# Kernel optimization log

Measured on AMD Instinct MI355X. Metric: run time of the kernel, lower is better.

The kernel has to match this reference:

```python
import jax, jax.numpy as jnp
import numpy as np

EMBED = 1024
FF = 4096
LN_EPS = 1e-5

def _layernorm(x, gamma, beta):
    mu = jnp.mean(x, axis=-1, keepdims=True)
    var = jnp.var(x, axis=-1, keepdims=True)
    return (x - mu) * jax.lax.rsqrt(var + LN_EPS) * gamma + beta

def setup_inputs() -> dict:
    key = jax.random.key(0)
    ks = jax.random.split(key, 16)
    s = 1.0 / np.sqrt(EMBED)
    s2 = 1.0 / np.sqrt(FF)
    return {
        "x": jax.random.normal(ks[0], (8, 2048, EMBED), dtype=jnp.float32),
        "Wq": jax.random.uniform(ks[1], (EMBED, EMBED), jnp.float32, -s, s),
        "bq": jnp.zeros((EMBED,), jnp.float32),
        "Wk": jax.random.uniform(ks[2], (EMBED, EMBED), jnp.float32, -s, s),
        "bk": jnp.zeros((EMBED,), jnp.float32),
        "Wv": jax.random.uniform(ks[3], (EMBED, EMBED), jnp.float32, -s, s),
        "bv": jnp.zeros((EMBED,), jnp.float32),
        "Wo": jax.random.uniform(ks[4], (EMBED, EMBED), jnp.float32, -s, s),
        "bo": jnp.zeros((EMBED,), jnp.float32),
        "g1": jnp.ones((EMBED,), jnp.float32),
        "b1": jnp.zeros((EMBED,), jnp.float32),
        "g2": jnp.ones((EMBED,), jnp.float32),
        "b2": jnp.zeros((EMBED,), jnp.float32),
        "W1": jax.random.uniform(ks[5], (EMBED, FF), jnp.float32, -s, s),
        "bf1": jnp.zeros((FF,), jnp.float32),
        "W2": jax.random.uniform(ks[6], (FF, EMBED), jnp.float32, -s2, s2),
        "bf2": jnp.zeros((EMBED,), jnp.float32),
    }

def reference(x, Wq, bq, Wk, bk, Wv, bv, Wo, bo, g1, b1, g2, b2, W1, bf1, W2, bf2):
    # Single-head attention (heads arg unused in original forward)
    Q = jnp.einsum('bse,ef->bsf', x, Wq) + bq
    K = jnp.einsum('bse,ef->bsf', x, Wk) + bk
    V = jnp.einsum('bse,ef->bsf', x, Wv) + bv
    scale = 1.0 / jnp.sqrt(jnp.float32(EMBED))
    scores = jnp.einsum('bqe,bke->bqk', Q, K) * scale  # [B,S,S]
    attn = jax.nn.softmax(scores, axis=-1)
    attn_out = jnp.einsum('bqk,bke->bqe', attn, V)
    attn_out = jnp.einsum('bse,ef->bsf', attn_out, Wo) + bo
    # dropout is identity in eval mode
    h = _layernorm(x + attn_out, g1, b1)
    ffn = jnp.einsum('bsf,fh->bsh', jax.nn.relu(jnp.einsum('bse,eh->bsh', h, W1) + bf1), W2) + bf2
    return _layernorm(h + ffn, g2, b2)
```

## Files before the change

### kernel.cpp

```cpp
#include <hip/hip_runtime.h>


typedef __attribute__((ext_vector_type(4))) float  f32x4;
typedef __attribute__((ext_vector_type(8))) short  s16x8;
typedef __attribute__((ext_vector_type(4))) short  s16x4;
typedef unsigned short u16;
typedef unsigned int   u32;

__device__ __forceinline__ float bf2f(short s) {
  u32 u = ((u32)(u16)s) << 16;
  float f; __builtin_memcpy(&f, &u, 4); return f;
}
__device__ __forceinline__ short f2bf(float f) {
  u32 u; __builtin_memcpy(&u, &f, 4);
  u32 r = (u + 0x7fffu + ((u >> 16) & 1u)) >> 16;
  return (short)(u16)r;
}

__device__ __forceinline__ void gload16(const void* g, void* l) {
  __builtin_amdgcn_global_load_lds(
      (const __attribute__((address_space(1))) u32*)g,
      (__attribute__((address_space(3))) u32*)l, 16, 0, 0);
}


__device__ __forceinline__ void stage_half(const char* gop, long long ldb,
                                           long long rowbase, int tt, int h,
                                           u16* ldsop, int tid) {
#pragma unroll
  for (int l = 0; l < 2; ++l) {
    const int o   = (l * 512 + tid) * 16;
    const int rih = o >> 7;
    const int scb = (o & 127) ^ ((rih & 7) << 4);
    gload16(gop + (rowbase + h * 128 + rih) * ldb + (long long)tt * 128 + scb,
            (char*)ldsop + h * 16384 + o);
  }
}

#define RD_A(MH) do { _Pragma("unroll") for (int mi = 0; mi < 4; ++mi) { \
    const int row_ = wm * 64 + (MH) * 128 + mi * 16 + lr; \
    const int sw_ = (row_ & 7) << 4; const int rb_ = row_ << 7; \
    _Pragma("unroll") for (int kk = 0; kk < 2; ++kk) \
      af[mi][kk] = *(const s16x8*)(pa + rb_ + (((kk << 6) | (kg << 4)) ^ sw_)); } } while (0)

#define RD_B(NH) do { _Pragma("unroll") for (int nj = 0; nj < 2; ++nj) { \
    const int row_ = wn * 32 + (NH) * 128 + nj * 16 + lr; \
    const int sw_ = (row_ & 7) << 4; const int rb_ = row_ << 7; \
    _Pragma("unroll") for (int kk = 0; kk < 2; ++kk) \
      bf[NH][nj][kk] = *(const s16x8*)(pb + rb_ + (((kk << 6) | (kg << 4)) ^ sw_)); } } while (0)

#define MM(MH, NH) do { _Pragma("unroll") for (int kk = 0; kk < 2; ++kk) \
    _Pragma("unroll") for (int mi = 0; mi < 4; ++mi) \
    _Pragma("unroll") for (int nj = 0; nj < 2; ++nj) \
      acc[(MH) * 4 + mi][(NH) * 2 + nj] = __builtin_amdgcn_mfma_f32_16x16x32_bf16( \
        af[mi][kk], bf[NH][nj][kk], acc[(MH) * 4 + mi][(NH) * 2 + nj], 0, 0, 0); } while (0)

#define PH_SYNC do { __builtin_amdgcn_s_barrier(); \
    asm volatile("s_waitcnt lgkmcnt(0)"); \
    __builtin_amdgcn_sched_barrier(0); } while (0)

template<int MODE>
__global__ __launch_bounds__(512, 2)
void gemm256(const u16* __restrict__ A, const u16* __restrict__ BT,
             u16* __restrict__ C,
             const float* __restrict__ bias0, const float* __restrict__ bias1,
             const float* __restrict__ bias2, const float* __restrict__ linv,
             int M, int N, int K, float scale,
             long long sA, long long sB, long long sC) {
  __shared__ u16 SA[2][16384];
  __shared__ u16 SB[2][16384];

  const int gx = gridDim.x, gy = gridDim.y;
  const int nwg = gx * gy * gridDim.z;
  const int orig = (blockIdx.z * gy + blockIdx.y) * gx + blockIdx.x;
  const int q = nwg >> 3, r8 = nwg & 7;
  const int xcd = orig & 7, pos = orig >> 3;
  const int wg = (xcd < r8 ? xcd * (q + 1) : r8 * (q + 1) + (xcd - r8) * q) + pos;
  const int bz = wg / (gx * gy);
  const int rem = wg % (gx * gy);
  const long long bm = (long long)(rem / gx) * 256;
  const long long bn = (long long)(rem % gx) * 256;

  const char* Ag = (const char*)(A + (long long)bz * sA);
  const char* Bg = (const char*)(BT + (long long)bz * sB);
  u16* Cb = C + (long long)bz * sC;
  const long long ldb = (long long)K * 2;

  const int tid = threadIdx.x;
  const int lane = tid & 63, wid = tid >> 6;
  const int lr = lane & 15, kg = lane >> 4;
  const int wm = wid >> 2, wn = wid & 3;
  const int NT = K >> 6;

  f32x4 acc[8][4] = {};
  s16x8 af[4][2];
  s16x8 bf[2][2][2];

  stage_half(Ag, ldb, bm, 0, 0, SA[0], tid);
  stage_half(Bg, ldb, bn, 0, 0, SB[0], tid);
  stage_half(Ag, ldb, bm, 0, 1, SA[0], tid);
  stage_half(Bg, ldb, bn, 0, 1, SB[0], tid);
  stage_half(Ag, ldb, bm, 1, 0, SA[1], tid);
  stage_half(Bg, ldb, bn, 1, 0, SB[1], tid);
  asm volatile("s_waitcnt vmcnt(4)");
  __builtin_amdgcn_s_barrier();

  for (int T = 0; T < NT; ++T) {
    const int c = T & 1, cn = c ^ 1;
    const char* pa = (const char*)SA[c];
    const char* pb = (const char*)SB[c];

    RD_A(0); RD_B(0);
    if (T + 1 < NT) stage_half(Ag, ldb, bm, T + 1, 1, SA[cn], tid);
    PH_SYNC;
    __builtin_amdgcn_s_setprio(1); MM(0, 0); __builtin_amdgcn_s_setprio(0);
    __builtin_amdgcn_s_barrier();

    RD_B(1);
    if (T + 1 < NT) stage_half(Bg, ldb, bn, T + 1, 1, SB[cn], tid);
    PH_SYNC;
    __builtin_amdgcn_s_setprio(1); MM(0, 1); __builtin_amdgcn_s_setprio(0);
    __builtin_amdgcn_s_barrier();

    RD_A(1);
    if (T + 2 < NT) stage_half(Ag, ldb, bm, T + 2, 0, SA[c], tid);
    PH_SYNC;
    __builtin_amdgcn_s_setprio(1); MM(1, 0); __builtin_amdgcn_s_setprio(0);
    __builtin_amdgcn_s_barrier();

    if (T + 2 < NT) stage_half(Bg, ldb, bn, T + 2, 0, SB[c], tid);
    PH_SYNC;
    __builtin_amdgcn_s_setprio(1); MM(1, 1); __builtin_amdgcn_s_setprio(0);
    if (T + 2 < NT)      { asm volatile("s_waitcnt vmcnt(4)"); }
    else if (T + 1 < NT) { asm volatile("s_waitcnt vmcnt(0)"); }
    __builtin_amdgcn_s_barrier();
  }

#pragma unroll
  for (int nh = 0; nh < 2; ++nh)
#pragma unroll
    for (int nj = 0; nj < 2; ++nj) {
      const long long col = bn + wn * 32 + nh * 128 + nj * 16 + lr;
      u16* outp = Cb;
      long long ccol = col, ldc = N;
      float bv = 0.f;
      if (MODE == 1 || MODE == 2) bv = bias0[col];
      if (MODE == 5) {
        const int sel = (int)(col >> 10);
        outp = C + (long long)sel * 16777216;
        ccol = col & 1023; ldc = 1024;
        bv = (sel == 0 ? bias0 : sel == 1 ? bias1 : bias2)[ccol];
      }
#pragma unroll
      for (int mh = 0; mh < 2; ++mh)
#pragma unroll
        for (int mi = 0; mi < 4; ++mi) {
          const long long row0 = bm + wm * 64 + mh * 128 + mi * 16 + kg * 4;
#pragma unroll
          for (int r = 0; r < 4; ++r) {
            float v = acc[mh * 4 + mi][nh * 2 + nj][r];
            if (MODE == 1 || MODE == 2 || MODE == 5) v = v * scale + bv;
            if (MODE == 2) v = fmaxf(v, 0.f);
            if (MODE == 3) v = __expf(v * scale);
            if (MODE == 4) v = v * linv[row0 + r];
            outp[(row0 + r) * ldc + ccol] = (u16)f2bf(v);
          }
        }
    }
}

__global__ __launch_bounds__(256) void cast_f32_bf16(const float* __restrict__ in,
                                                     u16* __restrict__ out) {
  long long i = (long long)blockIdx.x * 256 + threadIdx.x;
  f32x4 v = ((const f32x4*)in)[i];
  s16x4 o;
#pragma unroll
  for (int j = 0; j < 4; j++) o[j] = f2bf(v[j]);
  ((s16x4*)out)[i] = o;
}

__global__ __launch_bounds__(256) void transpose_f32_bf16(const float* __restrict__ in,
                                                          u16* __restrict__ out,
                                                          int R, int C) {
  __shared__ float tile[32][33];
  const int tx = threadIdx.x, ty = threadIdx.y;
  const int r0 = blockIdx.y * 32, c0 = blockIdx.x * 32;
#pragma unroll
  for (int i = 0; i < 32; i += 8)
    tile[ty + i][tx] = in[(long long)(r0 + ty + i) * C + (c0 + tx)];
  __syncthreads();
#pragma unroll
  for (int i = 0; i < 32; i += 8)
    out[(long long)(c0 + ty + i) * R + (r0 + tx)] = (u16)f2bf(tile[tx][ty + i]);
}

__global__ __launch_bounds__(256) void transpose_bf16_bf16(const u16* __restrict__ in,
                                                           u16* __restrict__ out,
                                                           int R, int C,
                                                           long long isb, long long osb) {
  __shared__ u16 tile[32][33];
  in  += (long long)blockIdx.z * isb;
  out += (long long)blockIdx.z * osb;
  const int tx = threadIdx.x, ty = threadIdx.y;
  const int r0 = blockIdx.y * 32, c0 = blockIdx.x * 32;
#pragma unroll
  for (int i = 0; i < 32; i += 8)
    tile[ty + i][tx] = in[(long long)(r0 + ty + i) * C + (c0 + tx)];
  __syncthreads();
#pragma unroll
  for (int i = 0; i < 32; i += 8)
    out[(long long)(c0 + ty + i) * R + (r0 + tx)] = tile[tx][ty + i];
}

__global__ __launch_bounds__(256) void rowinv2048(const u16* __restrict__ P,
                                                  float* __restrict__ linv) {
  const long long row = blockIdx.x;
  const u16* p = P + row * 2048;
  const int t = threadIdx.x;
  s16x8 raw = *(const s16x8*)&p[t * 8];
  float s = 0.f;
#pragma unroll
  for (int j = 0; j < 8; j++) s += bf2f(raw[j]);
#pragma unroll
  for (int off = 32; off > 0; off >>= 1) s += __shfl_xor(s, off);
  __shared__ float red[4];
  if ((t & 63) == 0) red[t >> 6] = s;
  __syncthreads();
  if (t == 0) {
    s = (red[0] + red[1]) + (red[2] + red[3]);
    linv[row] = 1.0f / s;
  }
}

__global__ __launch_bounds__(256) void ln_add_f32bf16(const float* __restrict__ x,
                                                      const u16* __restrict__ a,
                                                      const float* __restrict__ g,
                                                      const float* __restrict__ be,
                                                      u16* __restrict__ out) {
  const long long row = blockIdx.x;
  const int t = threadIdx.x;
  f32x4 xv = ((const f32x4*)(x + row * 1024))[t];
  s16x4 av = ((const s16x4*)(a + row * 1024))[t];
  float v[4]; float sum = 0.f, ss = 0.f;
#pragma unroll
  for (int j = 0; j < 4; j++) { v[j] = xv[j] + bf2f(av[j]); sum += v[j]; ss += v[j] * v[j]; }
#pragma unroll
  for (int off = 32; off > 0; off >>= 1) { sum += __shfl_xor(sum, off); ss += __shfl_xor(ss, off); }
  __shared__ float red[8];
  if ((t & 63) == 0) { red[t >> 6] = sum; red[4 + (t >> 6)] = ss; }
  __syncthreads();
  sum = (red[0] + red[1]) + (red[2] + red[3]);
  ss  = (red[4] + red[5]) + (red[6] + red[7]);
  const float mu   = sum * (1.f / 1024.f);
  const float var  = ss * (1.f / 1024.f) - mu * mu;
  const float rstd = rsqrtf(var + 1e-5f);
  s16x4 o;
#pragma unroll
  for (int j = 0; j < 4; j++) {
    const int c = t * 4 + j;
    o[j] = f2bf((v[j] - mu) * rstd * g[c] + be[c]);
  }
  *(s16x4*)&out[row * 1024 + t * 4] = o;
}

__global__ __launch_bounds__(256) void ln_add_bf16bf16(const u16* __restrict__ h,
                                                       const u16* __restrict__ f,
                                                       const float* __restrict__ g,
                                                       const float* __restrict__ be,
                                                       float* __restrict__ out) {
  const long long row = blockIdx.x;
  const int t = threadIdx.x;
  s16x4 hv = ((const s16x4*)(h + row * 1024))[t];
  s16x4 fv = ((const s16x4*)(f + row * 1024))[t];
  float v[4]; float sum = 0.f, ss = 0.f;
#pragma unroll
  for (int j = 0; j < 4; j++) { v[j] = bf2f(hv[j]) + bf2f(fv[j]); sum += v[j]; ss += v[j] * v[j]; }
#pragma unroll
  for (int off = 32; off > 0; off >>= 1) { sum += __shfl_xor(sum, off); ss += __shfl_xor(ss, off); }
  __shared__ float red[8];
  if ((t & 63) == 0) { red[t >> 6] = sum; red[4 + (t >> 6)] = ss; }
  __syncthreads();
  sum = (red[0] + red[1]) + (red[2] + red[3]);
  ss  = (red[4] + red[5]) + (red[6] + red[7]);
  const float mu   = sum * (1.f / 1024.f);
  const float var  = ss * (1.f / 1024.f) - mu * mu;
  const float rstd = rsqrtf(var + 1e-5f);
  f32x4 o;
#pragma unroll
  for (int j = 0; j < 4; j++) {
    const int c = t * 4 + j;
    o[j] = (v[j] - mu) * rstd * g[c] + be[c];
  }
  ((f32x4*)(out + row * 1024))[t] = o;
}

extern "C" void kernel_launch(void* const* d_in, const int* in_sizes, int n_in,
                              void* d_out, int out_size, void* d_ws, size_t ws_size,
                              hipStream_t stream) {
  const float* x   = (const float*)d_in[0];
  const float* Wq  = (const float*)d_in[1];
  const float* bq  = (const float*)d_in[2];
  const float* Wk  = (const float*)d_in[3];
  const float* bk  = (const float*)d_in[4];
  const float* Wv  = (const float*)d_in[5];
  const float* bv  = (const float*)d_in[6];
  const float* Wo  = (const float*)d_in[7];
  const float* bo  = (const float*)d_in[8];
  const float* g1  = (const float*)d_in[9];
  const float* b1  = (const float*)d_in[10];
  const float* g2  = (const float*)d_in[11];
  const float* b2  = (const float*)d_in[12];
  const float* W1  = (const float*)d_in[13];
  const float* bf1 = (const float*)d_in[14];
  const float* W2  = (const float*)d_in[15];
  const float* bf2 = (const float*)d_in[16];
  float* out = (float*)d_out;

  char* ws = (char*)d_ws;
  u16* wsWQT = (u16*)(ws + 0);
  u16* wsWKT = (u16*)(ws + 2097152);
  u16* wsWVT = (u16*)(ws + 4194304);
  u16* wsWOT = (u16*)(ws + 6291456);
  u16* wsW1T = (u16*)(ws + 8388608);
  u16* wsW2T = (u16*)(ws + 16777216);
  u16* wsXB  = (u16*)(ws + 25165824);
  u16* wsQ   = (u16*)(ws + 58720256);
  u16* wsK   = (u16*)(ws + 92274688);
  u16* wsV   = (u16*)(ws + 125829120);
  u16* wsVT  = (u16*)(ws + 159383552);
  u16* wsS   = (u16*)(ws + 192937984);
  u16* wsAO  = wsXB;
  u16* wsAO2 = wsQ;
  u16* wsH   = wsK;
  u16* wsHID = wsV;
  u16* wsFFN = wsXB;
  float* wsLINV = (float*)wsQ;

  const dim3 tb(32, 8, 1);
  const float inv_sqrt_e = 0.03125f;
  const float* nf = nullptr;

  cast_f32_bf16<<<16384, 256, 0, stream>>>(x, wsXB);

  transpose_f32_bf16<<<dim3(32, 32, 1),  tb, 0, stream>>>(Wq, wsWQT, 1024, 1024);
  transpose_f32_bf16<<<dim3(32, 32, 1),  tb, 0, stream>>>(Wk, wsWKT, 1024, 1024);
  transpose_f32_bf16<<<dim3(32, 32, 1),  tb, 0, stream>>>(Wv, wsWVT, 1024, 1024);
  transpose_f32_bf16<<<dim3(32, 32, 1),  tb, 0, stream>>>(Wo, wsWOT, 1024, 1024);
  transpose_f32_bf16<<<dim3(128, 32, 1), tb, 0, stream>>>(W1, wsW1T, 1024, 4096);
  transpose_f32_bf16<<<dim3(32, 128, 1), tb, 0, stream>>>(W2, wsW2T, 4096, 1024);

  gemm256<5><<<dim3(12, 64, 1), 512, 0, stream>>>(wsXB, wsWQT, wsQ, bq, bk, bv, nf,
                                                  16384, 3072, 1024, 1.f, 0, 0, 0);

  transpose_bf16_bf16<<<dim3(32, 64, 8), tb, 0, stream>>>(wsV, wsVT, 2048, 1024, 2048LL * 1024, 1024LL * 2048);

  gemm256<3><<<dim3(8, 8, 8), 512, 0, stream>>>(wsQ, wsK, wsS, nf, nf, nf, nf,
                                                2048, 2048, 1024, inv_sqrt_e,
                                                2048LL * 1024, 2048LL * 1024, 2048LL * 2048);
  rowinv2048<<<16384, 256, 0, stream>>>(wsS, wsLINV);

  gemm256<4><<<dim3(4, 8, 8), 512, 0, stream>>>(wsS, wsVT, wsAO, nf, nf, nf, wsLINV,
                                                2048, 1024, 2048, 1.f,
                                                2048LL * 2048, 1024LL * 2048, 2048LL * 1024);
  gemm256<1><<<dim3(4, 64, 1), 512, 0, stream>>>(wsAO, wsWOT, wsAO2, bo, nf, nf, nf,
                                                 16384, 1024, 1024, 1.f, 0, 0, 0);

  ln_add_f32bf16<<<16384, 256, 0, stream>>>(x, wsAO2, g1, b1, wsH);

  gemm256<2><<<dim3(16, 64, 1), 512, 0, stream>>>(wsH, wsW1T, wsHID, bf1, nf, nf, nf,
                                                  16384, 4096, 1024, 1.f, 0, 0, 0);

  gemm256<1><<<dim3(4, 64, 1), 512, 0, stream>>>(wsHID, wsW2T, wsFFN, bf2, nf, nf, nf,
                                                 16384, 1024, 4096, 1.f, 0, 0, 0);

  ln_add_bf16bf16<<<16384, 256, 0, stream>>>(wsH, wsFFN, g2, b2, out);

  (void)in_sizes; (void)n_in; (void)out_size; (void)ws_size;
}
```

Before: 683.1 us.

## Make GEMM kernels persistent with cross-tile prefetch of next tile's operands

Replaces the one-block-per-tile GEMM with a persistent kernel launched with 256 workgroups. Each workgroup loops over tiles in an XCD-aware order and stages the next tile's first K-slices into LDS while it finishes the current tile. This removes launch and tail-wave overhead and the pipeline-fill bubble at each tile start. In exchange, the 256-block grid leaves only one workgroup per CU although launch bounds allow two, which reduces latency hiding, and the epilogue is no longer overlapped by another resident block. The softmax row-inverse lookup now also adds a batch offset.

Result: slower. 748.9 us (+9.6%).

```diff
diff --git a/kernel.cpp b/kernel.cpp
--- a/kernel.cpp
+++ b/kernel.cpp
@@ -22,7 +22,6 @@
       (const __attribute__((address_space(1))) u32*)g,
       (__attribute__((address_space(3))) u32*)l, 16, 0, 0);
 }
-
 
 __device__ __forceinline__ void stage_half(const char* gop, long long ldb,
                                            long long rowbase, int tt, int h,
@@ -59,114 +58,155 @@
     asm volatile("s_waitcnt lgkmcnt(0)"); \
     __builtin_amdgcn_sched_barrier(0); } while (0)
 
+__device__ __forceinline__ int perm8(int orig, int ntiles) {
+  const int q = ntiles >> 3, r8 = ntiles & 7;
+  const int xcd = orig & 7, pos = orig >> 3;
+  return (xcd < r8 ? xcd * (q + 1) : r8 * (q + 1) + (xcd - r8) * q) + pos;
+}
+
 template<int MODE>
 __global__ __launch_bounds__(512, 2)
-void gemm256(const u16* __restrict__ A, const u16* __restrict__ BT,
-             u16* __restrict__ C,
-             const float* __restrict__ bias0, const float* __restrict__ bias1,
-             const float* __restrict__ bias2, const float* __restrict__ linv,
-             int M, int N, int K, float scale,
-             long long sA, long long sB, long long sC) {
+void gemm256p(const u16* __restrict__ A, const u16* __restrict__ BT,
+              u16* __restrict__ C,
+              const float* __restrict__ bias0, const float* __restrict__ bias1,
+              const float* __restrict__ bias2, const float* __restrict__ linv,
+              int M, int N, int K, int NBZ,
+              long long sA, long long sB, long long sC, float scale) {
   __shared__ u16 SA[2][16384];
   __shared__ u16 SB[2][16384];
 
-  const int gx = gridDim.x, gy = gridDim.y;
-  const int nwg = gx * gy * gridDim.z;
-  const int orig = (blockIdx.z * gy + blockIdx.y) * gx + blockIdx.x;
-  const int q = nwg >> 3, r8 = nwg & 7;
-  const int xcd = orig & 7, pos = orig >> 3;
-  const int wg = (xcd < r8 ? xcd * (q + 1) : r8 * (q + 1) + (xcd - r8) * q) + pos;
-  const int bz = wg / (gx * gy);
-  const int rem = wg % (gx * gy);
-  const long long bm = (long long)(rem / gx) * 256;
-  const long long bn = (long long)(rem % gx) * 256;
-
-  const char* Ag = (const char*)(A + (long long)bz * sA);
-  const char* Bg = (const char*)(BT + (long long)bz * sB);
-  u16* Cb = C + (long long)bz * sC;
+  const int tn = N >> 8;
+  const int tilesPerZ = (M >> 8) * tn;
+  const int ntiles = NBZ * tilesPerZ;
+  const int NT = K >> 6;
   const long long ldb = (long long)K * 2;
+  const int G = gridDim.x;
 
   const int tid = threadIdx.x;
   const int lane = tid & 63, wid = tid >> 6;
   const int lr = lane & 15, kg = lane >> 4;
   const int wm = wid >> 2, wn = wid & 3;
-  const int NT = K >> 6;
+
+  const char *curA, *curB, *nxtA, *nxtB;
+  long long curBm, curBn, nxtBm, nxtBn;
+  int curZ, nxtZ;
+  auto mk = [&](int tl, const char*& ag, const char*& bg,
+                long long& bm, long long& bn, int& z) {
+    z = tl / tilesPerZ;
+    const int rm = tl - z * tilesPerZ;
+    bm = (long long)(rm / tn) << 8;
+    bn = (long long)(rm - (rm / tn) * tn) << 8;
+    ag = (const char*)(A + (long long)z * sA);
+    bg = (const char*)(BT + (long long)z * sB);
+  };
+
+  int jt = blockIdx.x;
+  mk(perm8(jt, ntiles), curA, curB, curBm, curBn, curZ);
+  bool hasNext = (jt + G) < ntiles;
+  if (hasNext) mk(perm8(jt + G, ntiles), nxtA, nxtB, nxtBm, nxtBn, nxtZ);
+  else { nxtA = curA; nxtB = curB; nxtBm = curBm; nxtBn = curBn; nxtZ = curZ; }
 
   f32x4 acc[8][4] = {};
   s16x8 af[4][2];
   s16x8 bf[2][2][2];
 
-  stage_half(Ag, ldb, bm, 0, 0, SA[0], tid);
-  stage_half(Bg, ldb, bn, 0, 0, SB[0], tid);
-  stage_half(Ag, ldb, bm, 0, 1, SA[0], tid);
-  stage_half(Bg, ldb, bn, 0, 1, SB[0], tid);
-  stage_half(Ag, ldb, bm, 1, 0, SA[1], tid);
-  stage_half(Bg, ldb, bn, 1, 0, SB[1], tid);
+  stage_half(curA, ldb, curBm, 0, 0, SA[0], tid);
+  stage_half(curB, ldb, curBn, 0, 0, SB[0], tid);
+  stage_half(curA, ldb, curBm, 0, 1, SA[0], tid);
+  stage_half(curB, ldb, curBn, 0, 1, SB[0], tid);
+  stage_half(curA, ldb, curBm, 1, 0, SA[1], tid);
+  stage_half(curB, ldb, curBn, 1, 0, SB[1], tid);
   asm volatile("s_waitcnt vmcnt(4)");
   __builtin_amdgcn_s_barrier();
 
-  for (int T = 0; T < NT; ++T) {
-    const int c = T & 1, cn = c ^ 1;
-    const char* pa = (const char*)SA[c];
-    const char* pb = (const char*)SB[c];
-
-    RD_A(0); RD_B(0);
-    if (T + 1 < NT) stage_half(Ag, ldb, bm, T + 1, 1, SA[cn], tid);
-    PH_SYNC;
-    __builtin_amdgcn_s_setprio(1); MM(0, 0); __builtin_amdgcn_s_setprio(0);
-    __builtin_amdgcn_s_barrier();
-
-    RD_B(1);
-    if (T + 1 < NT) stage_half(Bg, ldb, bn, T + 1, 1, SB[cn], tid);
-    PH_SYNC;
-    __builtin_amdgcn_s_setprio(1); MM(0, 1); __builtin_amdgcn_s_setprio(0);
-    __builtin_amdgcn_s_barrier();
-
-    RD_A(1);
-    if (T + 2 < NT) stage_half(Ag, ldb, bm, T + 2, 0, SA[c], tid);
-    PH_SYNC;
-    __builtin_amdgcn_s_setprio(1); MM(1, 0); __builtin_amdgcn_s_setprio(0);
-    __builtin_amdgcn_s_barrier();
-
-    if (T + 2 < NT) stage_half(Bg, ldb, bn, T + 2, 0, SB[c], tid);
-    PH_SYNC;
-    __builtin_amdgcn_s_setprio(1); MM(1, 1); __builtin_amdgcn_s_setprio(0);
-    if (T + 2 < NT)      { asm volatile("s_waitcnt vmcnt(4)"); }
-    else if (T + 1 < NT) { asm volatile("s_waitcnt vmcnt(0)"); }
-    __builtin_amdgcn_s_barrier();
-  }
-
-#pragma unroll
-  for (int nh = 0; nh < 2; ++nh)
-#pragma unroll
-    for (int nj = 0; nj < 2; ++nj) {
-      const long long col = bn + wn * 32 + nh * 128 + nj * 16 + lr;
-      u16* outp = Cb;
-      long long ccol = col, ldc = N;
-      float bv = 0.f;
-      if (MODE == 1 || MODE == 2) bv = bias0[col];
-      if (MODE == 5) {
-        const int sel = (int)(col >> 10);
-        outp = C + (long long)sel * 16777216;
-        ccol = col & 1023; ldc = 1024;
-        bv = (sel == 0 ? bias0 : sel == 1 ? bias1 : bias2)[ccol];
-      }
-#pragma unroll
-      for (int mh = 0; mh < 2; ++mh)
-#pragma unroll
-        for (int mi = 0; mi < 4; ++mi) {
-          const long long row0 = bm + wm * 64 + mh * 128 + mi * 16 + kg * 4;
-#pragma unroll
-          for (int r = 0; r < 4; ++r) {
-            float v = acc[mh * 4 + mi][nh * 2 + nj][r];
-            if (MODE == 1 || MODE == 2 || MODE == 5) v = v * scale + bv;
-            if (MODE == 2) v = fmaxf(v, 0.f);
-            if (MODE == 3) v = __expf(v * scale);
-            if (MODE == 4) v = v * linv[row0 + r];
-            outp[(row0 + r) * ldc + ccol] = (u16)f2bf(v);
+  int vt = 0;
+  for (;;) {
+    for (int T = 0; T < NT; ++T, ++vt) {
+      const int c = vt & 1, cn = c ^ 1;
+      const char* pa = (const char*)SA[c];
+      const char* pb = (const char*)SB[c];
+
+      const bool in1 = (T + 1 < NT), in2 = (T + 2 < NT);
+      const bool v1 = in1 || hasNext, v2 = in2 || hasNext;
+      const char* a1 = in1 ? curA : nxtA;  const char* b1 = in1 ? curB : nxtB;
+      const long long m1 = in1 ? curBm : nxtBm, n1 = in1 ? curBn : nxtBn;
+      const int tk1 = in1 ? T + 1 : 0;
+      const char* a2 = in2 ? curA : nxtA;  const char* b2 = in2 ? curB : nxtB;
+      const long long m2 = in2 ? curBm : nxtBm, n2 = in2 ? curBn : nxtBn;
+      const int tk2 = in2 ? T + 2 : T + 2 - NT;
+
+      RD_A(0); RD_B(0);
+      if (v1) stage_half(a1, ldb, m1, tk1, 1, SA[cn], tid);
+      PH_SYNC;
+      __builtin_amdgcn_s_setprio(1); MM(0, 0); __builtin_amdgcn_s_setprio(0);
+      __builtin_amdgcn_s_barrier();
+
+      RD_B(1);
+      if (v1) stage_half(b1, ldb, n1, tk1, 1, SB[cn], tid);
+      PH_SYNC;
+      __builtin_amdgcn_s_setprio(1); MM(0, 1); __builtin_amdgcn_s_setprio(0);
+      __builtin_amdgcn_s_barrier();
+
+      RD_A(1);
+      if (v2) stage_half(a2, ldb, m2, tk2, 0, SA[c], tid);
+      PH_SYNC;
+      __builtin_amdgcn_s_setprio(1); MM(1, 0); __builtin_amdgcn_s_setprio(0);
+      __builtin_amdgcn_s_barrier();
+
+      if (v2) stage_half(b2, ldb, n2, tk2, 0, SB[c], tid);
+      PH_SYNC;
+      __builtin_amdgcn_s_setprio(1); MM(1, 1); __builtin_amdgcn_s_setprio(0);
+      if (v2)      { asm volatile("s_waitcnt vmcnt(4)"); }
+      else if (v1) { asm volatile("s_waitcnt vmcnt(0)"); }
+      __builtin_amdgcn_s_barrier();
+    }
+
+    {
+      u16* Cb = C + (long long)curZ * sC;
+      const long long zM = (long long)curZ * M;
+#pragma unroll
+      for (int nh = 0; nh < 2; ++nh)
+#pragma unroll
+        for (int nj = 0; nj < 2; ++nj) {
+          const long long col = curBn + wn * 32 + nh * 128 + nj * 16 + lr;
+          u16* outp = Cb;
+          long long ccol = col, ldc = N;
+          float bv = 0.f;
+          if (MODE == 1 || MODE == 2) bv = bias0[col];
+          if (MODE == 5) {
+            const int sel = (int)(col >> 10);
+            outp = C + (long long)sel * 16777216;
+            ccol = col & 1023; ldc = 1024;
+            bv = (sel == 0 ? bias0 : sel == 1 ? bias1 : bias2)[ccol];
           }
+#pragma unroll
+          for (int mh = 0; mh < 2; ++mh)
+#pragma unroll
+            for (int mi = 0; mi < 4; ++mi) {
+              const long long row0 = curBm + wm * 64 + mh * 128 + mi * 16 + kg * 4;
+#pragma unroll
+              for (int r = 0; r < 4; ++r) {
+                float v = acc[mh * 4 + mi][nh * 2 + nj][r];
+                if (MODE == 1 || MODE == 2 || MODE == 5) v = v * scale + bv;
+                if (MODE == 2) v = fmaxf(v, 0.f);
+                if (MODE == 3) v = __expf(v * scale);
+                if (MODE == 4) v = v * linv[zM + row0 + r];
+                outp[(row0 + r) * ldc + ccol] = (u16)f2bf(v);
+              }
+            }
         }
     }
+
+    jt += G;
+    if (jt >= ntiles) break;
+    curA = nxtA; curB = nxtB; curBm = nxtBm; curBn = nxtBn; curZ = nxtZ;
+    hasNext = (jt + G) < ntiles;
+    if (hasNext) mk(perm8(jt + G, ntiles), nxtA, nxtB, nxtBm, nxtBn, nxtZ);
+#pragma unroll
+    for (int i = 0; i < 8; ++i)
+#pragma unroll
+      for (int j = 0; j < 4; ++j) acc[i][j] = (f32x4){0.f, 0.f, 0.f, 0.f};
+  }
 }
 
 __global__ __launch_bounds__(256) void cast_f32_bf16(const float* __restrict__ in,
@@ -349,29 +389,29 @@
   transpose_f32_bf16<<<dim3(128, 32, 1), tb, 0, stream>>>(W1, wsW1T, 1024, 4096);
   transpose_f32_bf16<<<dim3(32, 128, 1), tb, 0, stream>>>(W2, wsW2T, 4096, 1024);
 
-  gemm256<5><<<dim3(12, 64, 1), 512, 0, stream>>>(wsXB, wsWQT, wsQ, bq, bk, bv, nf,
-                                                  16384, 3072, 1024, 1.f, 0, 0, 0);
+  gemm256p<5><<<256, 512, 0, stream>>>(wsXB, wsWQT, wsQ, bq, bk, bv, nf,
+                                       16384, 3072, 1024, 1, 0, 0, 0, 1.f);
 
   transpose_bf16_bf16<<<dim3(32, 64, 8), tb, 0, stream>>>(wsV, wsVT, 2048, 1024, 2048LL * 1024, 1024LL * 2048);
 
-  gemm256<3><<<dim3(8, 8, 8), 512, 0, stream>>>(wsQ, wsK, wsS, nf, nf, nf, nf,
-                                                2048, 2048, 1024, inv_sqrt_e,
-                                                2048LL * 1024, 2048LL * 1024, 2048LL * 2048);
+  gemm256p<3><<<256, 512, 0, stream>>>(wsQ, wsK, wsS, nf, nf, nf, nf,
+                                       2048, 2048, 1024, 8,
+                                       2048LL * 1024, 2048LL * 1024, 2048LL * 2048, inv_sqrt_e);
   rowinv2048<<<16384, 256, 0, stream>>>(wsS, wsLINV);
 
-  gemm256<4><<<dim3(4, 8, 8), 512, 0, stream>>>(wsS, wsVT, wsAO, nf, nf, nf, wsLINV,
-                                                2048, 1024, 2048, 1.f,
-                                                2048LL * 2048, 1024LL * 2048, 2048LL * 1024);
-  gemm256<1><<<dim3(4, 64, 1), 512, 0, stream>>>(wsAO, wsWOT, wsAO2, bo, nf, nf, nf,
-                                                 16384, 1024, 1024, 1.f, 0, 0, 0);
+  gemm256p<4><<<256, 512, 0, stream>>>(wsS, wsVT, wsAO, nf, nf, nf, wsLINV,
+                                       2048, 1024, 2048, 8,
+                                       2048LL * 2048, 1024LL * 2048, 2048LL * 1024, 1.f);
+  gemm256p<1><<<256, 512, 0, stream>>>(wsAO, wsWOT, wsAO2, bo, nf, nf, nf,
+                                       16384, 1024, 1024, 1, 0, 0, 0, 1.f);
 
   ln_add_f32bf16<<<16384, 256, 0, stream>>>(x, wsAO2, g1, b1, wsH);
 
-  gemm256<2><<<dim3(16, 64, 1), 512, 0, stream>>>(wsH, wsW1T, wsHID, bf1, nf, nf, nf,
-                                                  16384, 4096, 1024, 1.f, 0, 0, 0);
-
-  gemm256<1><<<dim3(4, 64, 1), 512, 0, stream>>>(wsHID, wsW2T, wsFFN, bf2, nf, nf, nf,
-                                                 16384, 1024, 4096, 1.f, 0, 0, 0);
+  gemm256p<2><<<256, 512, 0, stream>>>(wsH, wsW1T, wsHID, bf1, nf, nf, nf,
+                                       16384, 4096, 1024, 1, 0, 0, 0, 1.f);
+
+  gemm256p<1><<<256, 512, 0, stream>>>(wsHID, wsW2T, wsFFN, bf2, nf, nf, nf,
+                                       16384, 1024, 4096, 1, 0, 0, 0, 1.f);
 
   ln_add_bf16bf16<<<16384, 256, 0, stream>>>(wsH, wsFFN, g2, b2, out);
 
```
